# Optimization experiments

Hardware: AMD Instinct MI355X
Metric: run time of the kernel (lower is better)

## Reference

```python
import jax, jax.numpy as jnp
from jax import lax
import numpy as np

DIM = 384; NH = 8; N = 16; K = 4; DIN = 768; DTR = 24  # d_model, heads, d_state, d_conv, d_inner, dt_rank
B = 8; Hh = 48; Ww = 48


def _ln(x, g, b):
    m = jnp.mean(x, -1, keepdims=True)
    v = jnp.mean((x - m) ** 2, -1, keepdims=True)
    return (x - m) / jnp.sqrt(v + 1e-5) * g + b


def _mamba(x, in_w, in_b, conv_w, conv_b, xp_w, dt_w, dt_b, A_log, Dp, out_w, out_b):
    # x: (B, L, DIM)
    Bb, L, _ = x.shape
    xz = x @ in_w.T + in_b                      # (B, L, 2*DIN)
    xm, z = xz[..., :DIN], xz[..., DIN:]
    # depthwise causal conv over sequence
    xc = jnp.pad(xm.transpose(0, 2, 1), ((0, 0), (0, 0), (K - 1, 0)))  # (B, DIN, L+K-1)
    xconv = lax.conv_general_dilated(xc, conv_w[:, None, :], (1,), 'VALID',
                                     feature_group_count=DIN,
                                     dimension_numbers=('NCH', 'OIH', 'NCH'))
    u = jax.nn.silu((xconv + conv_b[None, :, None]).transpose(0, 2, 1))  # (B, L, DIN)
    dbc = u @ xp_w.T                            # (B, L, DTR + 2N)
    delta = jax.nn.softplus(dbc[..., :DTR] @ dt_w.T + dt_b)  # (B, L, DIN)
    Bm = dbc[..., DTR:DTR + N]                  # (B, L, N)
    Cm = dbc[..., DTR + N:]                     # (B, L, N)
    A = -jnp.exp(A_log)                         # (DIN, N)

    def step(h, inp):
        d_t, B_t, C_t, u_t = inp                # (B,DIN),(B,N),(B,N),(B,DIN)
        dA = jnp.exp(d_t[:, :, None] * A)       # (B, DIN, N)
        h = h * dA + d_t[:, :, None] * B_t[:, None, :] * u_t[:, :, None]
        y = jnp.einsum('bdn,bn->bd', h, C_t)
        return h, y

    h0 = jnp.zeros((Bb, DIN, N), x.dtype)
    xs = (delta.transpose(1, 0, 2), Bm.transpose(1, 0, 2), Cm.transpose(1, 0, 2), u.transpose(1, 0, 2))
    _, ys = lax.scan(step, h0, xs)
    y = ys.transpose(1, 0, 2) + u * Dp
    y = y * jax.nn.silu(z)
    return y @ out_w.T + out_b


def _forward(x, n1_g, n1_b, ap_w, ap_b, n2_g, n2_b, in_w, in_b, conv_w, conv_b, xp_w, dt_w, dt_b,
             A_log, Dp, out_w, out_b, mod_w1, mod_b1, mod_w2, mod_b2, n3_g, n3_b,
             fc1_w, fc1_b, fc2_w, fc2_b):
    Bb, C, Hc, Wc = x.shape
    xs = x.reshape(Bb, C, Hc * Wc).transpose(0, 2, 1)          # (B, L, C)
    xn = _ln(xs, n1_g, n1_b)
    attn = jax.nn.softmax(xn @ ap_w.T + ap_b, axis=1)          # softmax over sequence
    gc = jnp.einsum('bln,blc->bnc', attn, xn).mean(1)          # (B, C)
    mod = jax.nn.silu(gc @ mod_w1.T + mod_b1) @ mod_w2.T + mod_b2
    xn2 = _ln(xs, n2_g, n2_b)
    mo = _mamba(xn2, in_w, in_b, conv_w, conv_b, xp_w, dt_w, dt_b, A_log, Dp, out_w, out_b)
    mo = mo * (1.0 + mod[:, None, :])
    xs = xs + mo
    h = _ln(xs, n3_g, n3_b)
    h = jax.nn.gelu(h @ fc1_w.T + fc1_b) @ fc2_w.T + fc2_b
    xs = xs + h
    return xs.transpose(0, 2, 1).reshape(Bb, C, Hc, Wc)


def setup_inputs() -> dict:
    key = jax.random.key(0)
    ks = jax.random.split(key, 16)
    s = 0.02
    p = {}
    p['x'] = jax.random.normal(ks[0], (B, DIM, Hh, Ww), jnp.float32)
    p['n1_g'] = jnp.ones((DIM,), jnp.float32); p['n1_b'] = jnp.zeros((DIM,), jnp.float32)
    p['ap_w'] = jax.random.normal(ks[1], (NH, DIM), jnp.float32) * s; p['ap_b'] = jnp.zeros((NH,), jnp.float32)
    p['n2_g'] = jnp.ones((DIM,), jnp.float32); p['n2_b'] = jnp.zeros((DIM,), jnp.float32)
    p['in_w'] = jax.random.normal(ks[2], (2 * DIN, DIM), jnp.float32) * s; p['in_b'] = jnp.zeros((2 * DIN,), jnp.float32)
    p['conv_w'] = jax.random.normal(ks[3], (DIN, K), jnp.float32) * s; p['conv_b'] = jnp.zeros((DIN,), jnp.float32)
    p['xp_w'] = jax.random.normal(ks[4], (DTR + 2 * N, DIN), jnp.float32) * s
    p['dt_w'] = jax.random.normal(ks[5], (DIN, DTR), jnp.float32) * s
    p['dt_b'] = jax.random.uniform(ks[6], (DIN,), jnp.float32, minval=-4.0, maxval=-2.0)
    p['A_log'] = jnp.log(jnp.tile(jnp.arange(1, N + 1, dtype=jnp.float32), (DIN, 1)))
    p['Dp'] = jnp.ones((DIN,), jnp.float32)
    p['out_w'] = jax.random.normal(ks[7], (DIM, DIN), jnp.float32) * s; p['out_b'] = jnp.zeros((DIM,), jnp.float32)
    p['mod_w1'] = jax.random.normal(ks[8], (2 * DIM, DIM), jnp.float32) * s; p['mod_b1'] = jnp.zeros((2 * DIM,), jnp.float32)
    p['mod_w2'] = jax.random.normal(ks[9], (DIM, 2 * DIM), jnp.float32) * s; p['mod_b2'] = jnp.zeros((DIM,), jnp.float32)
    p['n3_g'] = jnp.ones((DIM,), jnp.float32); p['n3_b'] = jnp.zeros((DIM,), jnp.float32)
    p['fc1_w'] = jax.random.normal(ks[10], (4 * DIM, DIM), jnp.float32) * s; p['fc1_b'] = jnp.zeros((4 * DIM,), jnp.float32)
    p['fc2_w'] = jax.random.normal(ks[11], (DIM, 4 * DIM), jnp.float32) * s; p['fc2_b'] = jnp.zeros((DIM,), jnp.float32)
    return p


def reference(x, n1_g, n1_b, ap_w, ap_b, n2_g, n2_b, in_w, in_b, conv_w, conv_b, xp_w, dt_w, dt_b,
              A_log, Dp, out_w, out_b, mod_w1, mod_b1, mod_w2, mod_b2, n3_g, n3_b,
              fc1_w, fc1_b, fc2_w, fc2_b):
    return _forward(x, n1_g, n1_b, ap_w, ap_b, n2_g, n2_b, in_w, in_b, conv_w, conv_b, xp_w,
                    dt_w, dt_b, A_log, Dp, out_w, out_b, mod_w1, mod_b1, mod_w2, mod_b2,
                    n3_g, n3_b, fc1_w, fc1_b, fc2_w, fc2_b)
```

## Files before the change

### kernel.cpp

```cpp
#include <hip/hip_runtime.h>
#include <math.h>

#define DIMC 384
#define NHD 8
#define NSTATE 16
#define DINN 768
#define DTRK 24
#define BB 8
#define LSEQ 2304
#define MROWS (BB*LSEQ)
#define NCH 64
#define TCH 36
#define L2E 1.44269504f

typedef unsigned short u16;
typedef short bf16x8 __attribute__((ext_vector_type(8)));
typedef float f32x4 __attribute__((ext_vector_type(4)));

__device__ __forceinline__ float sigmoid_(float x){ return 1.f/(1.f+__expf(-x)); }
__device__ __forceinline__ float silu_(float x){ return x*sigmoid_(x); }
__device__ __forceinline__ float softplus_(float x){ return (x>20.f)?x:log1pf(__expf(x)); }
__device__ __forceinline__ float gelu_(float x){
  float x3=x*x*x;
  return 0.5f*x*(1.f+tanhf(0.7978845608028654f*(x+0.044715f*x3)));
}
__device__ __forceinline__ float bfu2f(u16 u){
  union{unsigned int i; float f;} c; c.i=((unsigned int)u)<<16; return c.f;
}
__device__ __forceinline__ u16 f2bfu(float f){
  union{float f; unsigned int i;} c; c.f=f;
  unsigned int r = c.i + 0x7FFFu + ((c.i>>16)&1u);
  return (u16)(r>>16);
}
__device__ __forceinline__ void gl_lds16(const u16* g, u16* l){
  __builtin_amdgcn_global_load_lds((__attribute__((address_space(1))) void*)g,
      (__attribute__((address_space(3))) void*)l, 16, 0, 0);
}

__global__ void k_cvt(const float* __restrict__ s, u16* __restrict__ d, int n){
  int i=blockIdx.x*256+threadIdx.x; if(i<n) d[i]=f2bfu(s[i]);
}
__global__ void k_cvtpad(const float* __restrict__ s, u16* __restrict__ d, int nsrc, int ntot){
  int i=blockIdx.x*256+threadIdx.x; if(i<ntot) d[i] = (i<nsrc)? f2bfu(s[i]) : (u16)0;
}

__global__ void k_transpose(const float* __restrict__ x, float* __restrict__ xs){
  __shared__ float tile[32][33];
  int b = blockIdx.z;
  int t0 = blockIdx.x*32, c0 = blockIdx.y*32;
  int tx = threadIdx.x, ty = threadIdx.y;
  const float* xb = x + (size_t)b*DIMC*LSEQ;
  #pragma unroll
  for(int q=0;q<4;q++)
    tile[ty+q*8][tx] = xb[(size_t)(c0+ty+q*8)*LSEQ + t0+tx];
  __syncthreads();
  float* xsb = xs + (size_t)b*LSEQ*DIMC;
  #pragma unroll
  for(int q=0;q<4;q++)
    xsb[(size_t)(t0+ty+q*8)*DIMC + c0+tx] = tile[tx][ty+q*8];
}

__global__ __launch_bounds__(64) void k_lnstats(const float* __restrict__ xs,
   const float* __restrict__ g1,const float* __restrict__ b1,
   const float* __restrict__ g2,const float* __restrict__ b2,
   const float* __restrict__ apw,const float* __restrict__ apb,
   float* __restrict__ meanr, float* __restrict__ rstdr,
   u16* __restrict__ xn2, float* __restrict__ scores){
  int row = blockIdx.x;
  int lane = threadIdx.x;
  const float* xr = xs + (size_t)row*DIMC;
  float v[6];
  float s=0.f, s2=0.f;
  #pragma unroll
  for(int i=0;i<6;i++){ v[i]=xr[lane+i*64]; s+=v[i]; s2+=v[i]*v[i]; }
  #pragma unroll
  for(int m=32;m>=1;m>>=1){ s += __shfl_xor(s,m); s2 += __shfl_xor(s2,m); }
  float mean = s*(1.f/DIMC);
  float var  = s2*(1.f/DIMC)-mean*mean;
  float rstd = rsqrtf(var+1e-5f);
  if(lane==0){ meanr[row]=mean; rstdr[row]=rstd; }
  float xv1[6];
  #pragma unroll
  for(int i=0;i<6;i++){
    int c = lane+i*64;
    float nx = (v[i]-mean)*rstd;
    xv1[i] = nx*g1[c]+b1[c];
    xn2[(size_t)row*DIMC+c] = f2bfu(nx*g2[c]+b2[c]);
  }
  #pragma unroll
  for(int h=0;h<NHD;h++){
    float p=0.f;
    #pragma unroll
    for(int i=0;i<6;i++) p += xv1[i]*apw[h*DIMC+lane+i*64];
    #pragma unroll
    for(int m=32;m>=1;m>>=1) p += __shfl_xor(p,m);
    if(lane==0) scores[(size_t)row*NHD+h]=p+apb[h];
  }
}

__global__ __launch_bounds__(256) void k_softmax_L(float* __restrict__ sc){
  int bh = blockIdx.x; int b = bh>>3, h = bh&7;
  int tid = threadIdx.x;
  __shared__ float red[8];
  const size_t base = (size_t)b*LSEQ*NHD + h;
  float mx = -1e30f;
  for(int l=tid;l<LSEQ;l+=256) mx = fmaxf(mx, sc[base + (size_t)l*NHD]);
  #pragma unroll
  for(int m=32;m>=1;m>>=1) mx = fmaxf(mx, __shfl_xor(mx,m));
  if((tid&63)==0) red[tid>>6]=mx;
  __syncthreads();
  mx = fmaxf(fmaxf(red[0],red[1]),fmaxf(red[2],red[3]));
  float sum=0.f;
  for(int l=tid;l<LSEQ;l+=256) sum += __expf(sc[base+(size_t)l*NHD]-mx);
  #pragma unroll
  for(int m=32;m>=1;m>>=1) sum += __shfl_xor(sum,m);
  if((tid&63)==0) red[4+(tid>>6)]=sum;
  __syncthreads();
  float inv = 1.f/(red[4]+red[5]+red[6]+red[7]);
  for(int l=tid;l<LSEQ;l+=256){
    size_t idx = base+(size_t)l*NHD;
    sc[idx] = __expf(sc[idx]-mx)*inv;
  }
}

__global__ void k_wpool(const float* __restrict__ attn, float* __restrict__ w){
  int i = blockIdx.x*256+threadIdx.x;
  if(i<MROWS){
    const float* a = attn+(size_t)i*NHD;
    float s=0.f;
    #pragma unroll
    for(int h=0;h<NHD;h++) s+=a[h];
    w[i]=s*0.125f;
  }
}

__global__ void k_zero(float* __restrict__ p, int n){
  int i=blockIdx.x*256+threadIdx.x; if(i<n)p[i]=0.f;
}

__global__ __launch_bounds__(384) void k_gc(const float* __restrict__ w,
    const float* __restrict__ xs, const float* __restrict__ meanr,
    const float* __restrict__ rstdr, const float* __restrict__ g1,
    const float* __restrict__ b1, float* __restrict__ gc){
  int b = blockIdx.x; int chunk = blockIdx.y; int c = threadIdx.x;
  int l0 = chunk*192;
  float acc=0.f, accw=0.f;
  for(int l=0;l<192;l++){
    int row = b*LSEQ + l0+l;
    float ww = w[row];
    acc  += ww*(xs[(size_t)row*DIMC+c]-meanr[row])*rstdr[row];
    accw += ww;
  }
  atomicAdd(&gc[b*DIMC+c], acc*g1[c]+accw*b1[c]);
}

__global__ __launch_bounds__(64) void k_mod1(const float* __restrict__ gc,
    const float* __restrict__ w1, const float* __restrict__ b1, float* __restrict__ h){
  int b = blockIdx.x; int n = blockIdx.y*64+threadIdx.x;
  const float* g = gc + b*DIMC;
  const float* wr = w1 + (size_t)n*DIMC;
  float acc=0.f;
  for(int k=0;k<DIMC;k++) acc += g[k]*wr[k];
  h[b*768+n] = silu_(acc+b1[n]);
}
__global__ __launch_bounds__(64) void k_mod2(const float* __restrict__ h,
    const float* __restrict__ w2, const float* __restrict__ b2, float* __restrict__ mod){
  int b = blockIdx.x; int n = blockIdx.y*64+threadIdx.x;
  const float* hh = h + b*768;
  const float* wr = w2 + (size_t)n*768;
  float acc=0.f;
  for(int k=0;k<768;k++) acc += hh[k]*wr[k];
  mod[b*DIMC+n] = acc+b2[n];
}

template<int EPI>
__global__ __launch_bounds__(256,2) void k_mgemm(
    const u16* __restrict__ A, const u16* __restrict__ W,
    const float* __restrict__ bias, void* __restrict__ outp,
    int K, int N, const float* __restrict__ aux, void* __restrict__ outp2)
{
  __shared__ u16 lA[2][4096];
  __shared__ u16 lB[2][4096];
  int tid = threadIdx.x;
  int m0 = blockIdx.x*128, n0 = blockIdx.y*128;
  int wid = tid>>6, lane = tid&63;
  int wr = wid>>1, wc = wid&1;
  int lrow = lane&15, lk = lane>>4;
  f32x4 acc[4][4];
  #pragma unroll
  for(int i=0;i<4;i++)
    #pragma unroll
    for(int j=0;j<4;j++){ acc[i][j][0]=0.f; acc[i][j][1]=0.f; acc[i][j][2]=0.f; acc[i][j][3]=0.f; }

  int r0 = tid & 127, k0 = tid >> 7;
  const u16* Ag0 = A + (size_t)(m0+r0)*K + k0*8;
  const u16* Ag1 = A + (size_t)(m0+r0)*K + (k0+2)*8;
  const u16* Bg0 = W + (size_t)(n0+r0)*K + k0*8;
  const u16* Bg1 = W + (size_t)(n0+r0)*K + (k0+2)*8;

  gl_lds16(Ag0, &lA[0][tid*8]);
  gl_lds16(Ag1, &lA[0][2048+tid*8]);
  gl_lds16(Bg0, &lB[0][tid*8]);
  gl_lds16(Bg1, &lB[0][2048+tid*8]);
  __syncthreads();

  int cur = 0;
  for(int kb=0; kb<K; kb+=32){
    if(kb+32 < K){
      int nb = cur^1;
      gl_lds16(Ag0 + kb+32, &lA[nb][tid*8]);
      gl_lds16(Ag1 + kb+32, &lA[nb][2048+tid*8]);
      gl_lds16(Bg0 + kb+32, &lB[nb][tid*8]);
      gl_lds16(Bg1 + kb+32, &lB[nb][2048+tid*8]);
    }
    bf16x8 af[4], bfr[4];
    #pragma unroll
    for(int i=0;i<4;i++){
      af[i]  = *reinterpret_cast<const bf16x8*>(&lA[cur][(lk*128 + wr*64 + i*16 + lrow)*8]);
      bfr[i] = *reinterpret_cast<const bf16x8*>(&lB[cur][(lk*128 + wc*64 + i*16 + lrow)*8]);
    }
    #pragma unroll
    for(int i=0;i<4;i++)
      #pragma unroll
      for(int j=0;j<4;j++)
        acc[i][j] = __builtin_amdgcn_mfma_f32_16x16x32_bf16(af[i], bfr[j], acc[i][j], 0,0,0);
    __syncthreads();
    cur ^= 1;
  }

  #pragma unroll
  for(int i=0;i<4;i++){
    int row = m0 + wr*64 + i*16 + lk*4;
    #pragma unroll
    for(int j=0;j<4;j++){
      int col = n0 + wc*64 + j*16 + lrow;
      float bc = bias ? bias[col] : 0.f;
      f32x4 v = acc[i][j];
      if(EPI==0){
        u16* o = (u16*)outp;
        #pragma unroll
        for(int r=0;r<4;r++) o[(size_t)(row+r)*N + col] = f2bfu(v[r]+bc);
      } else if(EPI==1){
        u16* o = (u16*)outp;
        #pragma unroll
        for(int r=0;r<4;r++) o[(size_t)(row+r)*N + col] = f2bfu(gelu_(v[r]+bc));
      } else if(EPI==2){
        float* o = (float*)outp;
        int bi = row/LSEQ;
        float sc = 1.f + aux[bi*DIMC + col];
        #pragma unroll
        for(int r=0;r<4;r++) o[(size_t)(row+r)*DIMC + col] += (v[r]+bc)*sc;
      } else if(EPI==3){
        float* o = (float*)outp;
        int bi = row/LSEQ, t = row - bi*LSEQ;
        float4 s;
        s.x = aux[(size_t)(row+0)*DIMC+col] + v[0] + bc;
        s.y = aux[(size_t)(row+1)*DIMC+col] + v[1] + bc;
        s.z = aux[(size_t)(row+2)*DIMC+col] + v[2] + bc;
        s.w = aux[(size_t)(row+3)*DIMC+col] + v[3] + bc;
        *reinterpret_cast<float4*>(&o[((size_t)(bi*DIMC+col))*LSEQ + t]) = s;
      } else if(EPI==4){
        float* o = (float*)outp;
        if(col < N){
          #pragma unroll
          for(int r=0;r<4;r++) o[(size_t)(row+r)*N + col] = v[r]+bc;
        }
      } else {
        u16* o = (col < 768) ? (u16*)outp : (u16*)outp2;
        int cc = (col < 768) ? col : col - 768;
        #pragma unroll
        for(int r=0;r<4;r++) o[(size_t)(row+r)*768 + cc] = f2bfu(v[r]+bc);
      }
    }
  }
}

__global__ void k_conv(const u16* __restrict__ xm, const float* __restrict__ cw,
                       const float* __restrict__ cb, u16* __restrict__ u){
  int idx = blockIdx.x*256+threadIdx.x;
  if(idx >= MROWS*(DINN/8)) return;
  int j = idx % (DINN/8); int r = idx / (DINN/8);
  int t = r % LSEQ; int d0 = j*8;
  float4 w4_[8];
  #pragma unroll
  for(int e=0;e<8;e++) w4_[e] = reinterpret_cast<const float4*>(cw)[d0+e];
  float acc[8];
  #pragma unroll
  for(int e=0;e<8;e++) acc[e]=cb[d0+e];
  #pragma unroll
  for(int k=0;k<4;k++){
    int tt=t+k-3;
    if(tt>=0){
      uint4 v = *reinterpret_cast<const uint4*>(&xm[(size_t)(r+k-3)*DINN + d0]);
      unsigned vv[4]={v.x,v.y,v.z,v.w};
      #pragma unroll
      for(int e=0;e<8;e++){
        u16 raw = (e&1)? (u16)(vv[e>>1]>>16) : (u16)(vv[e>>1]&0xffffu);
        float wk = (k==0)? w4_[e].x : (k==1)? w4_[e].y : (k==2)? w4_[e].z : w4_[e].w;
        acc[e] += bfu2f(raw)*wk;
      }
    }
  }
  u16 outv[8];
  #pragma unroll
  for(int e=0;e<8;e++) outv[e]=f2bfu(silu_(acc[e]));
  *reinterpret_cast<uint4*>(&u[(size_t)r*DINN+d0]) = *reinterpret_cast<const uint4*>(outv);
}

__global__ __launch_bounds__(256) void k_dtgemm(const float* __restrict__ DBC,
    const float* __restrict__ dtw, const float* __restrict__ dtb,
    u16* __restrict__ delta){
  __shared__ float As[64][24];
  __shared__ float Ws[64][24];
  int tid = threadIdx.x;
  int m0 = blockIdx.x*64, n0 = blockIdx.y*64;
  for(int j=tid;j<64*24;j+=256){
    int rr=j/24, kk=j-rr*24;
    As[rr][kk]=DBC[(size_t)(m0+rr)*56+kk];
    Ws[rr][kk]=dtw[(size_t)(n0+rr)*24+kk];
  }
  __syncthreads();
  int tx=tid&15, ty=tid>>4;
  float acc[4][4]={};
  for(int k=0;k<24;k++){
    float a[4],w[4];
    #pragma unroll
    for(int i=0;i<4;i++){a[i]=As[ty*4+i][k]; w[i]=Ws[tx*4+i][k];}
    #pragma unroll
    for(int i=0;i<4;i++)
      #pragma unroll
      for(int j=0;j<4;j++) acc[i][j]+=a[i]*w[j];
  }
  #pragma unroll
  for(int i=0;i<4;i++){
    int row=m0+ty*4+i;
    #pragma unroll
    for(int j=0;j<4;j++){
      int col=n0+tx*4+j;
      delta[(size_t)row*DINN+col]=f2bfu(softplus_(acc[i][j]+dtb[col]));
    }
  }
}

__global__ __launch_bounds__(256) void k_scan1(
  const u16* __restrict__ dt_, const u16* __restrict__ u_,
  const float* __restrict__ dbc, const float* __restrict__ alog,
  float* __restrict__ ssum, float* __restrict__ hloc)
{
  __shared__ float Bsh[TCH][16];
  int bid = blockIdx.x;
  int b = bid/(NCH*3); int rem = bid%(NCH*3); int ch = rem/3; int dblk = rem%3;
  int tid = threadIdx.x; int d = dblk*256 + tid;
  size_t rbase = (size_t)b*LSEQ + (size_t)ch*TCH;
  for(int j=tid; j<TCH*16; j+=256){
    int row=j>>4, n=j&15;
    Bsh[row][n] = dbc[(rbase+row)*56 + DTRK + n];
  }
  float Acl2[16];
  float a0 = -__expf(alog[(size_t)d*16])*L2E;
  bool fast = true;
  #pragma unroll
  for(int n=0;n<16;n++){
    Acl2[n] = -__expf(alog[(size_t)d*16+n])*L2E;
    float tgt = (float)(n+1)*a0;
    fast = fast && (fabsf(Acl2[n]-tgt) <= 1e-4f*fabsf(tgt));
  }
  float h[16];
  #pragma unroll
  for(int n=0;n<16;n++) h[n]=0.f;
  float S=0.f;
  const u16* dtp = dt_ + rbase*DINN + d;
  const u16* up  = u_  + rbase*DINN + d;
  __syncthreads();
  if(fast){
    for(int t=0;t<TCH;t++){
      float dt = bfu2f(dtp[(size_t)t*DINN]);
      float uv = bfu2f(up[(size_t)t*DINN]);
      float G = dt*uv;
      S += dt;
      float e = exp2f(dt*a0), w = e;
      const float4* b4 = (const float4*)Bsh[t];
      float4 B0=b4[0],B1=b4[1],B2=b4[2],B3=b4[3];
      float Bv[16]={B0.x,B0.y,B0.z,B0.w,B1.x,B1.y,B1.z,B1.w,
                    B2.x,B2.y,B2.z,B2.w,B3.x,B3.y,B3.z,B3.w};
      #pragma unroll
      for(int n=0;n<16;n++){ h[n] = h[n]*w + G*Bv[n]; w *= e; }
    }
  } else {
    for(int t=0;t<TCH;t++){
      float dt = bfu2f(dtp[(size_t)t*DINN]);
      float uv = bfu2f(up[(size_t)t*DINN]);
      float G = dt*uv;
      S += dt;
      const float4* b4 = (const float4*)Bsh[t];
      float4 B0=b4[0],B1=b4[1],B2=b4[2],B3=b4[3];
      float Bv[16]={B0.x,B0.y,B0.z,B0.w,B1.x,B1.y,B1.z,B1.w,
                    B2.x,B2.y,B2.z,B2.w,B3.x,B3.y,B3.z,B3.w};
      #pragma unroll
      for(int n=0;n<16;n++) h[n] = h[n]*exp2f(dt*Acl2[n]) + G*Bv[n];
    }
  }
  ssum[((size_t)b*NCH+ch)*DINN + d] = S;
  float* hp = hloc + (((size_t)b*NCH+ch)*DINN + d)*16;
  #pragma unroll
  for(int n=0;n<16;n++) hp[n] = h[n];
}

__global__ __launch_bounds__(256) void k_scan2(
  const float* __restrict__ ssum, const float* __restrict__ alog,
  float* __restrict__ hl)
{
  int gid = blockIdx.x*256+threadIdx.x;
  int n = gid & 15; int d = (gid>>4)%DINN; int b = gid/(DINN*NSTATE);
  float Acl2 = -__expf(alog[(size_t)d*16+n])*L2E;
  float hin=0.f;
  for(int ch=0; ch<NCH; ch++){
    size_t sidx = ((size_t)b*NCH+ch)*DINN + d;
    size_t idx  = sidx*16 + n;
    float a = exp2f(ssum[sidx]*Acl2);
    float hold = hl[idx];
    hl[idx] = hin;
    hin = a*hin + hold;
  }
}

__global__ __launch_bounds__(256) void k_scan3(
  const u16* __restrict__ dt_, u16* uy, const u16* __restrict__ z_,
  const float* __restrict__ dbc, const float* __restrict__ alog,
  const float* __restrict__ Dp, const float* __restrict__ hin)
{
  __shared__ float BC[TCH][32];
  int bid = blockIdx.x;
  int b = bid/(NCH*3); int rem = bid%(NCH*3); int ch = rem/3; int dblk = rem%3;
  int tid = threadIdx.x; int d = dblk*256 + tid;
  size_t rbase = (size_t)b*LSEQ + (size_t)ch*TCH;
  for(int j=tid; j<TCH*32; j+=256){
    int row=j>>5, c=j&31;
    BC[row][c] = dbc[(rbase+row)*56 + DTRK + c];
  }
  float Acl2[16], h[16];
  const float* hp = hin + (((size_t)b*NCH+ch)*DINN + d)*16;
  float a0 = -__expf(alog[(size_t)d*16])*L2E;
  bool fast = true;
  #pragma unroll
  for(int n=0;n<16;n++){
    Acl2[n] = -__expf(alog[(size_t)d*16+n])*L2E;
    float tgt = (float)(n+1)*a0;
    fast = fast && (fabsf(Acl2[n]-tgt) <= 1e-4f*fabsf(tgt));
    h[n] = hp[n];
  }
  float Dv = Dp[d];
  const u16* dtp = dt_ + rbase*DINN + d;
  u16*       uyp = uy  + rbase*DINN + d;
  const u16* zp  = z_  + rbase*DINN + d;
  __syncthreads();
  if(fast){
    for(int t=0;t<TCH;t++){
      float dt = bfu2f(dtp[(size_t)t*DINN]);
      float uv = bfu2f(uyp[(size_t)t*DINN]);
      float zv = bfu2f(zp[(size_t)t*DINN]);
      float G = dt*uv;
      float e = exp2f(dt*a0), w = e;
      const float4* bc4 = (const float4*)BC[t];
      float4 B0=bc4[0],B1=bc4[1],B2=bc4[2],B3=bc4[3];
      float4 C0=bc4[4],C1=bc4[5],C2=bc4[6],C3=bc4[7];
      float Bv[16]={B0.x,B0.y,B0.z,B0.w,B1.x,B1.y,B1.z,B1.w,
                    B2.x,B2.y,B2.z,B2.w,B3.x,B3.y,B3.z,B3.w};
      float Cv[16]={C0.x,C0.y,C0.z,C0.w,C1.x,C1.y,C1.z,C1.w,
                    C2.x,C2.y,C2.z,C2.w,C3.x,C3.y,C3.z,C3.w};
      float y0=0.f,y1=0.f,y2=0.f,y3=0.f;
      #pragma unroll
      for(int n=0;n<16;n++){
        h[n] = h[n]*w + G*Bv[n];
        w *= e;
        if((n&3)==0) y0 += h[n]*Cv[n];
        else if((n&3)==1) y1 += h[n]*Cv[n];
        else if((n&3)==2) y2 += h[n]*Cv[n];
        else y3 += h[n]*Cv[n];
      }
      float y = (y0+y1)+(y2+y3);
      uyp[(size_t)t*DINN] = f2bfu((y + uv*Dv)*silu_(zv));
    }
  } else {
    for(int t=0;t<TCH;t++){
      float dt = bfu2f(dtp[(size_t)t*DINN]);
      float uv = bfu2f(uyp[(size_t)t*DINN]);
      float zv = bfu2f(zp[(size_t)t*DINN]);
      float G = dt*uv;
      const float4* bc4 = (const float4*)BC[t];
      float4 B0=bc4[0],B1=bc4[1],B2=bc4[2],B3=bc4[3];
      float4 C0=bc4[4],C1=bc4[5],C2=bc4[6],C3=bc4[7];
      float Bv[16]={B0.x,B0.y,B0.z,B0.w,B1.x,B1.y,B1.z,B1.w,
                    B2.x,B2.y,B2.z,B2.w,B3.x,B3.y,B3.z,B3.w};
      float Cv[16]={C0.x,C0.y,C0.z,C0.w,C1.x,C1.y,C1.z,C1.w,
                    C2.x,C2.y,C2.z,C2.w,C3.x,C3.y,C3.z,C3.w};
      float y0=0.f,y1=0.f,y2=0.f,y3=0.f;
      #pragma unroll
      for(int n=0;n<16;n++){
        h[n] = h[n]*exp2f(dt*Acl2[n]) + G*Bv[n];
        if((n&3)==0) y0 += h[n]*Cv[n];
        else if((n&3)==1) y1 += h[n]*Cv[n];
        else if((n&3)==2) y2 += h[n]*Cv[n];
        else y3 += h[n]*Cv[n];
      }
      float y = (y0+y1)+(y2+y3);
      uyp[(size_t)t*DINN] = f2bfu((y + uv*Dv)*silu_(zv));
    }
  }
}

__global__ __launch_bounds__(64) void k_ln3(const float* __restrict__ xin,
    const float* __restrict__ g, const float* __restrict__ bb, u16* __restrict__ xout){
  int row = blockIdx.x;
  int lane = threadIdx.x;
  const float* xr = xin + (size_t)row*DIMC;
  float v[6];
  float s=0.f, s2=0.f;
  #pragma unroll
  for(int i=0;i<6;i++){ v[i]=xr[lane+i*64]; s+=v[i]; s2+=v[i]*v[i]; }
  #pragma unroll
  for(int m=32;m>=1;m>>=1){ s += __shfl_xor(s,m); s2 += __shfl_xor(s2,m); }
  float mean = s*(1.f/DIMC);
  float var  = s2*(1.f/DIMC)-mean*mean;
  float rstd = rsqrtf(var+1e-5f);
  #pragma unroll
  for(int i=0;i<6;i++){
    int c = lane+i*64;
    xout[(size_t)row*DIMC+c] = f2bfu((v[i]-mean)*rstd*g[c]+bb[c]);
  }
}

extern "C" void kernel_launch(void* const* d_in, const int* in_sizes, int n_in,
                              void* d_out, int out_size, void* d_ws, size_t ws_size,
                              hipStream_t stream)
{
  const float* x     = (const float*)d_in[0];
  const float* n1g   = (const float*)d_in[1];
  const float* n1b   = (const float*)d_in[2];
  const float* apw   = (const float*)d_in[3];
  const float* apb   = (const float*)d_in[4];
  const float* n2g   = (const float*)d_in[5];
  const float* n2b   = (const float*)d_in[6];
  const float* inw   = (const float*)d_in[7];
  const float* inb   = (const float*)d_in[8];
  const float* convw = (const float*)d_in[9];
  const float* convb = (const float*)d_in[10];
  const float* xpw   = (const float*)d_in[11];
  const float* dtw   = (const float*)d_in[12];
  const float* dtb   = (const float*)d_in[13];
  const float* Alog  = (const float*)d_in[14];
  const float* Dp    = (const float*)d_in[15];
  const float* outw  = (const float*)d_in[16];
  const float* outb  = (const float*)d_in[17];
  const float* modw1 = (const float*)d_in[18];
  const float* modb1 = (const float*)d_in[19];
  const float* modw2 = (const float*)d_in[20];
  const float* modb2 = (const float*)d_in[21];
  const float* n3g   = (const float*)d_in[22];
  const float* n3b   = (const float*)d_in[23];
  const float* fc1w  = (const float*)d_in[24];
  const float* fc1b  = (const float*)d_in[25];
  const float* fc2w  = (const float*)d_in[26];
  const float* fc2b  = (const float*)d_in[27];

  float* ws = (float*)d_ws;
  float* XS    = ws;
  float* R1    = ws + 7077888;
  u16*   XMb   = (u16*)R1;
  u16*   DTb   = (u16*)R1;
  float* SSUM  = R1 + 7077888;
  float* HL    = R1 + 7471104;
  u16*   F1b   = (u16*)R1;
  u16*   Zb    = (u16*)(ws + 21233664);
  float* DBC   = ws + 28311552;
  float* WB    = ws + 29343744;
  u16*   inw_b   = (u16*)WB;
  u16*   xpw_pad = inw_b + 589824;
  u16*   outw_b  = xpw_pad + 98304;
  u16*   fc1w_b  = outw_b + 294912;
  u16*   fc2w_b  = fc1w_b + 589824;
  float* SCORES= ws + 30425088;
  float* WPOOL = ws + 30572544;
  float* MEANR = ws + 30590976;
  float* RSTDR = ws + 30609408;
  float* GC    = ws + 30627840;
  float* MODH  = ws + 30630912;
  float* MOD   = ws + 30637056;
  (void)ws_size; (void)n_in; (void)in_sizes; (void)out_size;

  u16* XN2b = (u16*)d_out;
  u16* Ub   = (u16*)d_out;
  u16* Hb   = (u16*)d_out;

  k_cvt<<<(589824+255)/256, 256, 0, stream>>>(inw,  inw_b,  589824);
  k_cvtpad<<<(98304+255)/256, 256, 0, stream>>>(xpw, xpw_pad, 56*768, 128*768);
  k_cvt<<<(294912+255)/256, 256, 0, stream>>>(outw, outw_b, 294912);
  k_cvt<<<(589824+255)/256, 256, 0, stream>>>(fc1w, fc1w_b, 589824);
  k_cvt<<<(589824+255)/256, 256, 0, stream>>>(fc2w, fc2w_b, 589824);

  k_transpose<<<dim3(72,12,8), dim3(32,8), 0, stream>>>(x, XS);
  k_lnstats<<<MROWS, 64, 0, stream>>>(XS, n1g,n1b,n2g,n2b, apw,apb, MEANR, RSTDR, XN2b, SCORES);
  k_softmax_L<<<BB*NHD, 256, 0, stream>>>(SCORES);
  k_wpool<<<(MROWS+255)/256, 256, 0, stream>>>(SCORES, WPOOL);
  k_zero<<<(BB*DIMC+255)/256, 256, 0, stream>>>(GC, BB*DIMC);
  k_gc<<<dim3(BB,12), 384, 0, stream>>>(WPOOL, XS, MEANR, RSTDR, n1g, n1b, GC);
  k_mod1<<<dim3(BB,12), 64, 0, stream>>>(GC, modw1, modb1, MODH);
  k_mod2<<<dim3(BB,6), 64, 0, stream>>>(MODH, modw2, modb2, MOD);

  k_mgemm<5><<<dim3(144,12), 256, 0, stream>>>(XN2b, inw_b, inb, XMb, 384, 1536, nullptr, Zb);
  k_conv<<<(MROWS*(DINN/8)+255)/256, 256, 0, stream>>>(XMb, convw, convb, Ub);
  k_mgemm<4><<<dim3(144,1), 256, 0, stream>>>(Ub, xpw_pad, nullptr, DBC, 768, 56, nullptr, nullptr);
  k_dtgemm<<<dim3(288,12), 256, 0, stream>>>(DBC, dtw, dtb, DTb);
  k_scan1<<<BB*NCH*3, 256, 0, stream>>>(DTb, Ub, DBC, Alog, SSUM, HL);
  k_scan2<<<384, 256, 0, stream>>>(SSUM, Alog, HL);
  k_scan3<<<BB*NCH*3, 256, 0, stream>>>(DTb, Ub, Zb, DBC, Alog, Dp, HL);
  k_mgemm<2><<<dim3(144,3), 256, 0, stream>>>(Ub, outw_b, outb, XS, 768, 384, MOD, nullptr);
  k_ln3<<<MROWS, 64, 0, stream>>>(XS, n3g, n3b, Hb);
  k_mgemm<1><<<dim3(144,12), 256, 0, stream>>>(Hb, fc1w_b, fc1b, F1b, 384, 1536, nullptr, nullptr);
  k_mgemm<3><<<dim3(144,3), 256, 0, stream>>>(F1b, fc2w_b, fc2b, d_out, 1536, 384, XS, nullptr);
}
```

Measured before the change: 571.4 us.

## Move dt projection to MFMA GEMM and merge weight conversions into one kernel

Replaces the scalar FP32 dt-projection GEMM with the bf16 MFMA GEMM template. The x_proj epilogue now also writes a K-padded (32-column) bf16 copy of the dt-rank slice, and a new epilogue applies softplus to the output. All weight conversions and the GC zeroing are merged into one launch, and k_gc gets four times as many blocks for more parallelism. This cuts launch overhead and moves the small-K GEMM onto matrix cores, at the cost of extra bf16 rounding of the dt inputs and more atomics in k_gc.

```diff
diff --git a/kernel.cpp b/kernel.cpp
--- a/kernel.cpp
+++ b/kernel.cpp
@@ -37,11 +37,29 @@
       (__attribute__((address_space(3))) void*)l, 16, 0, 0);
 }
 
-__global__ void k_cvt(const float* __restrict__ s, u16* __restrict__ d, int n){
-  int i=blockIdx.x*256+threadIdx.x; if(i<n) d[i]=f2bfu(s[i]);
-}
-__global__ void k_cvtpad(const float* __restrict__ s, u16* __restrict__ d, int nsrc, int ntot){
-  int i=blockIdx.x*256+threadIdx.x; if(i<ntot) d[i] = (i<nsrc)? f2bfu(s[i]) : (u16)0;
+#define O1 589824
+#define O2 688128
+#define O3 983040
+#define O4 1572864
+#define O5 2162688
+#define O6 2187264
+#define OEND 2190336
+__global__ void k_cvtall(const float* __restrict__ inw, const float* __restrict__ xpw,
+    const float* __restrict__ outw, const float* __restrict__ fc1w,
+    const float* __restrict__ fc2w, const float* __restrict__ dtw,
+    u16* __restrict__ inw_b, u16* __restrict__ xpw_pad, u16* __restrict__ outw_b,
+    u16* __restrict__ fc1w_b, u16* __restrict__ fc2w_b, u16* __restrict__ dtw_pad,
+    float* __restrict__ gc){
+  int i = blockIdx.x*256+threadIdx.x;
+  if(i >= OEND) return;
+  if(i < O1){ inw_b[i]=f2bfu(inw[i]); }
+  else if(i < O2){ int j=i-O1; xpw_pad[j] = (j<43008)? f2bfu(xpw[j]) : (u16)0; }
+  else if(i < O3){ int j=i-O2; outw_b[j]=f2bfu(outw[j]); }
+  else if(i < O4){ int j=i-O3; fc1w_b[j]=f2bfu(fc1w[j]); }
+  else if(i < O5){ int j=i-O4; fc2w_b[j]=f2bfu(fc2w[j]); }
+  else if(i < O6){ int j=i-O5; int r=j>>5, c=j&31;
+                   dtw_pad[j] = (c<DTRK)? f2bfu(dtw[r*DTRK+c]) : (u16)0; }
+  else { gc[i-O6]=0.f; }
 }
 
 __global__ void k_transpose(const float* __restrict__ x, float* __restrict__ xs){
@@ -134,18 +152,14 @@
   }
 }
 
-__global__ void k_zero(float* __restrict__ p, int n){
-  int i=blockIdx.x*256+threadIdx.x; if(i<n)p[i]=0.f;
-}
-
 __global__ __launch_bounds__(384) void k_gc(const float* __restrict__ w,
     const float* __restrict__ xs, const float* __restrict__ meanr,
     const float* __restrict__ rstdr, const float* __restrict__ g1,
     const float* __restrict__ b1, float* __restrict__ gc){
   int b = blockIdx.x; int chunk = blockIdx.y; int c = threadIdx.x;
-  int l0 = chunk*192;
+  int l0 = chunk*48;
   float acc=0.f, accw=0.f;
-  for(int l=0;l<192;l++){
+  for(int l=0;l<48;l++){
     int row = b*LSEQ + l0+l;
     float ww = w[row];
     acc  += ww*(xs[(size_t)row*DIMC+c]-meanr[row])*rstdr[row];
@@ -265,11 +279,24 @@
           #pragma unroll
           for(int r=0;r<4;r++) o[(size_t)(row+r)*N + col] = v[r]+bc;
         }
-      } else {
+      } else if(EPI==5){
         u16* o = (col < 768) ? (u16*)outp : (u16*)outp2;
         int cc = (col < 768) ? col : col - 768;
         #pragma unroll
         for(int r=0;r<4;r++) o[(size_t)(row+r)*768 + cc] = f2bfu(v[r]+bc);
+      } else if(EPI==6){
+        float* o = (float*)outp;
+        u16* o2 = (u16*)outp2;
+        #pragma unroll
+        for(int r=0;r<4;r++){
+          float val = v[r];
+          if(col < 56) o[(size_t)(row+r)*56 + col] = val;
+          if(col < 32) o2[(size_t)(row+r)*32 + col] = (col<DTRK)? f2bfu(val) : (u16)0;
+        }
+      } else {
+        u16* o = (u16*)outp;
+        #pragma unroll
+        for(int r=0;r<4;r++) o[(size_t)(row+r)*N + col] = f2bfu(softplus_(v[r]+bc));
       }
     }
   }
@@ -305,41 +332,6 @@
   #pragma unroll
   for(int e=0;e<8;e++) outv[e]=f2bfu(silu_(acc[e]));
   *reinterpret_cast<uint4*>(&u[(size_t)r*DINN+d0]) = *reinterpret_cast<const uint4*>(outv);
-}
-
-__global__ __launch_bounds__(256) void k_dtgemm(const float* __restrict__ DBC,
-    const float* __restrict__ dtw, const float* __restrict__ dtb,
-    u16* __restrict__ delta){
-  __shared__ float As[64][24];
-  __shared__ float Ws[64][24];
-  int tid = threadIdx.x;
-  int m0 = blockIdx.x*64, n0 = blockIdx.y*64;
-  for(int j=tid;j<64*24;j+=256){
-    int rr=j/24, kk=j-rr*24;
-    As[rr][kk]=DBC[(size_t)(m0+rr)*56+kk];
-    Ws[rr][kk]=dtw[(size_t)(n0+rr)*24+kk];
-  }
-  __syncthreads();
-  int tx=tid&15, ty=tid>>4;
-  float acc[4][4]={};
-  for(int k=0;k<24;k++){
-    float a[4],w[4];
-    #pragma unroll
-    for(int i=0;i<4;i++){a[i]=As[ty*4+i][k]; w[i]=Ws[tx*4+i][k];}
-    #pragma unroll
-    for(int i=0;i<4;i++)
-      #pragma unroll
-      for(int j=0;j<4;j++) acc[i][j]+=a[i]*w[j];
-  }
-  #pragma unroll
-  for(int i=0;i<4;i++){
-    int row=m0+ty*4+i;
-    #pragma unroll
-    for(int j=0;j<4;j++){
-      int col=n0+tx*4+j;
-      delta[(size_t)row*DINN+col]=f2bfu(softplus_(acc[i][j]+dtb[col]));
-    }
-  }
 }
 
 __global__ __launch_bounds__(256) void k_scan1(
@@ -586,31 +578,29 @@
   float* GC    = ws + 30627840;
   float* MODH  = ws + 30630912;
   float* MOD   = ws + 30637056;
+  u16*   DT32b = (u16*)(ws + 30640128);
+  u16*   dtw_pad=(u16*)(ws + 30935040);
   (void)ws_size; (void)n_in; (void)in_sizes; (void)out_size;
 
   u16* XN2b = (u16*)d_out;
   u16* Ub   = (u16*)d_out;
   u16* Hb   = (u16*)d_out;
 
-  k_cvt<<<(589824+255)/256, 256, 0, stream>>>(inw,  inw_b,  589824);
-  k_cvtpad<<<(98304+255)/256, 256, 0, stream>>>(xpw, xpw_pad, 56*768, 128*768);
-  k_cvt<<<(294912+255)/256, 256, 0, stream>>>(outw, outw_b, 294912);
-  k_cvt<<<(589824+255)/256, 256, 0, stream>>>(fc1w, fc1w_b, 589824);
-  k_cvt<<<(589824+255)/256, 256, 0, stream>>>(fc2w, fc2w_b, 589824);
+  k_cvtall<<<(OEND+255)/256, 256, 0, stream>>>(inw, xpw, outw, fc1w, fc2w, dtw,
+      inw_b, xpw_pad, outw_b, fc1w_b, fc2w_b, dtw_pad, GC);
 
   k_transpose<<<dim3(72,12,8), dim3(32,8), 0, stream>>>(x, XS);
   k_lnstats<<<MROWS, 64, 0, stream>>>(XS, n1g,n1b,n2g,n2b, apw,apb, MEANR, RSTDR, XN2b, SCORES);
   k_softmax_L<<<BB*NHD, 256, 0, stream>>>(SCORES);
   k_wpool<<<(MROWS+255)/256, 256, 0, stream>>>(SCORES, WPOOL);
-  k_zero<<<(BB*DIMC+255)/256, 256, 0, stream>>>(GC, BB*DIMC);
-  k_gc<<<dim3(BB,12), 384, 0, stream>>>(WPOOL, XS, MEANR, RSTDR, n1g, n1b, GC);
+  k_gc<<<dim3(BB,48), 384, 0, stream>>>(WPOOL, XS, MEANR, RSTDR, n1g, n1b, GC);
   k_mod1<<<dim3(BB,12), 64, 0, stream>>>(GC, modw1, modb1, MODH);
   k_mod2<<<dim3(BB,6), 64, 0, stream>>>(MODH, modw2, modb2, MOD);
 
   k_mgemm<5><<<dim3(144,12), 256, 0, stream>>>(XN2b, inw_b, inb, XMb, 384, 1536, nullptr, Zb);
   k_conv<<<(MROWS*(DINN/8)+255)/256, 256, 0, stream>>>(XMb, convw, convb, Ub);
-  k_mgemm<4><<<dim3(144,1), 256, 0, stream>>>(Ub, xpw_pad, nullptr, DBC, 768, 56, nullptr, nullptr);
-  k_dtgemm<<<dim3(288,12), 256, 0, stream>>>(DBC, dtw, dtb, DTb);
+  k_mgemm<6><<<dim3(144,1), 256, 0, stream>>>(Ub, xpw_pad, nullptr, DBC, 768, 56, nullptr, DT32b);
+  k_mgemm<7><<<dim3(144,6), 256, 0, stream>>>(DT32b, dtw_pad, dtb, DTb, 32, 768, nullptr, nullptr);
   k_scan1<<<BB*NCH*3, 256, 0, stream>>>(DTb, Ub, DBC, Alog, SSUM, HL);
   k_scan2<<<384, 256, 0, stream>>>(SSUM, Alog, HL);
   k_scan3<<<BB*NCH*3, 256, 0, stream>>>(DTb, Ub, Zb, DBC, Alog, Dp, HL);
```

After: 535.8 us. 1.07x faster.
